# Kernel optimization log

Hardware: AMD Instinct MI355X
Metric: run time of the kernel (lower is better)

The kernel has to match this reference:

```python
import jax, jax.numpy as jnp
import numpy as np

N = 100_000   # nodes
E = 3_200_000 # edges (avg degree 32)
IN = 256      # input feature dim


def setup_inputs() -> dict:
    key = jax.random.key(0)
    ks = jax.random.split(key, 10)
    w = lambda k, s: (jax.random.normal(k, s, jnp.float32) * 0.02)
    return {
        "x": jax.random.normal(ks[0], (N, IN), jnp.float32),
        "edge_index": jax.random.randint(ks[1], (2, E), 0, N, dtype=jnp.int32),
        "edge_attr": jax.random.normal(ks[2], (E, 1), jnp.float32),
        # conv1: ExpGraphConv(IN, 64, 128)
        "W1a": w(ks[3], (IN, 64)), "b1a": jnp.zeros((64,), jnp.float32),
        "W1b": w(ks[4], (IN + 64, 128)), "b1b": jnp.zeros((128,), jnp.float32),
        # conv2: ExpGraphConv(128, 32->hidden 64? per ctor (128, 32, 64)): msg hidden 32... kept as repo: hidden=32? Using (128,64) msg, (192,64) out per faithful cat structure
        "W2a": w(ks[5], (128, 64)), "b2a": jnp.zeros((64,), jnp.float32),
        "W2b": w(ks[6], (128 + 64, 64)), "b2b": jnp.zeros((64,), jnp.float32),
        # head
        "Wl1": w(ks[7], (64, 32)), "bl1": jnp.zeros((32,), jnp.float32),
        "Wl2": w(ks[8], (32, 1)), "bl2": jnp.zeros((1,), jnp.float32),
    }


def _mean_aggr(h, src, dst, n):
    # gather messages from source nodes, scatter-mean into destination nodes
    s = jax.ops.segment_sum(h[src], dst, num_segments=n)          # [N, d]
    cnt = jax.ops.segment_sum(jnp.ones((src.shape[0],), h.dtype), dst, num_segments=n)
    return s / jnp.maximum(cnt, 1.0)[:, None]


def _exp_graph_conv(x, src, dst, Wa, ba, Wb, bb):
    # message MLP on source features, mean aggregation, then linear on [x || aggr]
    h = x @ Wa + ba                                               # [N, hidden]
    m = _mean_aggr(h, src, dst, x.shape[0])                       # [N, hidden]
    return jnp.concatenate([x, m], axis=1) @ Wb + bb              # [N, out]


def reference(x, edge_index, edge_attr, W1a, b1a, W1b, b1b, W2a, b2a, W2b, b2b, Wl1, bl1, Wl2, bl2):
    src, dst = edge_index[0], edge_index[1]
    x = jax.nn.relu(_exp_graph_conv(x, src, dst, W1a, b1a, W1b, b1b))
    x = jax.nn.relu(_exp_graph_conv(x, src, dst, W2a, b2a, W2b, b2b))
    x = jax.nn.relu(x @ Wl1 + bl1)
    return x @ Wl2 + bl2
```

## Files before the change

### kernel.cpp

```cpp
#include <hip/hip_runtime.h>

#define IN_DIM 256
#define CAP 10240
#define EPB 4096

typedef _Float16 f16;
typedef _Float16 f16x8 __attribute__((ext_vector_type(8)));
typedef float f32x4 __attribute__((ext_vector_type(4)));
typedef unsigned u32x4 __attribute__((ext_vector_type(4)));
typedef unsigned u32x2 __attribute__((ext_vector_type(2)));


__global__ __launch_bounds__(256) void bucket_scatter_k(const int* __restrict__ srcp,
                                                        const int* __restrict__ dstp,
                                                        int* __restrict__ bcur,
                                                        unsigned* __restrict__ bedge, int E) {
    __shared__ int cnt[512], lstart[512], delta[512], fill[512];
    __shared__ int pfx[256];
    __shared__ unsigned spay[EPB];
    __shared__ unsigned char sbk[EPB];
    int tid = threadIdx.x;
    cnt[tid] = 0; cnt[tid + 256] = 0;
    fill[tid] = 0; fill[tid + 256] = 0;
    __syncthreads();
    size_t base = (size_t)blockIdx.x * EPB;
    int nloc = E - (int)base; if (nloc > EPB) nloc = EPB;
    int dreg[EPB / 256], sreg[EPB / 256];
#pragma unroll
    for (int j = 0; j < EPB / 256; j++) {
        int e = j * 256 + tid;
        if (e < nloc) {
            dreg[j] = dstp[base + e];
            sreg[j] = srcp[base + e];
            atomicAdd(&cnt[dreg[j] >> 8], 1);
        }
    }
    __syncthreads();
    int a0 = cnt[2 * tid], a1 = cnt[2 * tid + 1], s = a0 + a1;
    pfx[tid] = s;
    __syncthreads();
    for (int off = 1; off < 256; off <<= 1) {
        int t2 = (tid >= off) ? pfx[tid - off] : 0;
        __syncthreads();
        pfx[tid] += t2;
        __syncthreads();
    }
    int excl = pfx[tid] - s;
    lstart[2 * tid] = excl;
    lstart[2 * tid + 1] = excl + a0;
    int g0 = 0, g1 = 0;
    if (a0) g0 = atomicAdd(&bcur[2 * tid], a0);
    if (a1) g1 = atomicAdd(&bcur[2 * tid + 1], a1);
    delta[2 * tid]     = (2 * tid) * CAP + g0 - excl;
    delta[2 * tid + 1] = (2 * tid + 1) * CAP + g1 - (excl + a0);
    __syncthreads();
#pragma unroll
    for (int j = 0; j < EPB / 256; j++) {
        int e = j * 256 + tid;
        if (e < nloc) {
            int d = dreg[j], bk = d >> 8;
            int slot = lstart[bk] + atomicAdd(&fill[bk], 1);
            spay[slot] = (unsigned)sreg[j] | ((unsigned)(d & 255) << 17);
            sbk[slot] = (unsigned char)bk;
        }
    }
    __syncthreads();
    int mid = lstart[256];
#pragma unroll
    for (int j = 0; j < EPB / 256; j++) {
        int i = j * 256 + tid;
        if (i < nloc) {
            int bk = (int)sbk[i] | ((i >= mid) ? 256 : 0);
            int gp = i + delta[bk];
            if (gp < (bk + 1) * CAP)
                bedge[gp] = spay[i];
        }
    }
}

__global__ __launch_bounds__(256) void fine_sort_k(unsigned* __restrict__ bedge,
                                                   const int* __restrict__ bcur,
                                                   int2* __restrict__ ose, int Nn) {
    __shared__ int cnt[256], cur[256], pfx[256];
    __shared__ int sorted[CAP];
    int b = blockIdx.x, tid = threadIdx.x;
    int lo = b * CAP;
    int sz = bcur[b];
    if (sz > CAP) sz = CAP;
    cnt[tid] = 0;
    __syncthreads();
    for (int i = tid; i < sz; i += 256) atomicAdd(&cnt[bedge[lo + i] >> 17], 1);
    __syncthreads();
    int c = cnt[tid];
    pfx[tid] = c;
    __syncthreads();
    for (int off = 1; off < 256; off <<= 1) {
        int t2 = (tid >= off) ? pfx[tid - off] : 0;
        __syncthreads();
        pfx[tid] += t2;
        __syncthreads();
    }
    int excl = pfx[tid] - c;
    cur[tid] = excl;
    int node = b * 256 + tid;
    if (node < Nn) ose[node] = make_int2(lo + excl, lo + excl + c);
    __syncthreads();
    for (int i = tid; i < sz; i += 256) {
        unsigned v = bedge[lo + i];
        int slot = atomicAdd(&cur[v >> 17], 1);
        sorted[slot] = (int)(v & 0x1FFFFu);
    }
    __syncthreads();
    for (int i = tid; i < sz; i += 256) bedge[lo + i] = (unsigned)sorted[i];
}


__global__ __launch_bounds__(256) void prep_k(
    const float* __restrict__ W1a, const float* __restrict__ W1b,
    const float* __restrict__ W2a, const float* __restrict__ W2b,
    const float* __restrict__ b1a, const float* __restrict__ b1b,
    const float* __restrict__ b2a, const float* __restrict__ b2b,
    f16* __restrict__ Wt1, f16* __restrict__ Wt2,
    f16* __restrict__ Wmt1, f16* __restrict__ Wmt2,
    float* __restrict__ bc1, float* __restrict__ bc2,
    int* __restrict__ bcur) {
    int tid = threadIdx.x;
    if (blockIdx.x == 0) { bcur[tid] = 0; bcur[tid + 256] = 0; }
    int i = blockIdx.x * 256 + tid;
    if (i < 49152) {
        int n = i >> 8, k = i & 255;
        Wt1[i] = (f16)(n < 64 ? W1a[k * 64 + n] : W1b[k * 128 + (n - 64)]);
    } else if (i < 65536) {
        int l = i - 49152; int n = l >> 7, k = l & 127;
        Wt2[l] = (f16)(n < 64 ? W2a[k * 64 + n] : W2b[k * 64 + (n - 64)]);
    } else if (i < 73728) {
        int l = i - 65536; int n = l >> 6, k = l & 63;
        Wmt1[l] = (f16)W1b[(256 + k) * 128 + n];
    } else if (i < 77824) {
        int l = i - 73728; int n = l >> 6, k = l & 63;
        Wmt2[l] = (f16)W2b[(128 + k) * 64 + n];
    } else if (i < 78016) {
        int l = i - 77824; bc1[l] = l < 64 ? b1a[l] : b1b[l - 64];
    } else if (i < 78144) {
        int l = i - 78016; bc2[l] = l < 64 ? b2a[l] : b2b[l - 64];
    }
}


__global__ __launch_bounds__(256) void gemm_fused192(const float* __restrict__ A1,
                                                     const f16* __restrict__ Wt,
                                                     const float* __restrict__ bc,
                                                     f16* __restrict__ Y1,
                                                     f16* __restrict__ Y2, int M) {
    constexpr int BN = 192, BM = 64, BK = 32, ASTR = BK + 8, K1 = 256;
    constexpr int WN = BN / 2, NB = WN / 16, SEGB = BN / 64;
    constexpr int EPS = BN + 8, TPR = BN / 8;
    constexpr size_t SM_AB = (size_t)BM * ASTR * 2 + (size_t)BN * ASTR * 2;
    constexpr size_t SM_EP = (size_t)BM * EPS * 2;
    constexpr size_t SM = SM_AB > SM_EP ? SM_AB : SM_EP;
    __shared__ __align__(16) char smem[SM];
    f16* As = reinterpret_cast<f16*>(smem);
    f16* Bs = reinterpret_cast<f16*>(smem + (size_t)BM * ASTR * 2);
    const int tid  = threadIdx.x;
    const int wave = tid >> 6, lane = tid & 63;
    const int wr = wave >> 1, wc = wave & 1;
    const int quad = lane >> 4, l16 = lane & 15;
    const int row0 = blockIdx.x * BM;

    f32x4 acc[2][NB];
#pragma unroll
    for (int i = 0; i < 2; i++)
#pragma unroll
        for (int j = 0; j < NB; j++) acc[i][j] = (f32x4)(0.f);

    const int ra = tid >> 2, sa = tid & 3;
    int rowA = row0 + ra;  if (rowA >= M) rowA = M - 1;

    u32x4 aReg, bReg[SEGB];
    auto loadA = [&](int kk) {
        const float* bp = A1 + (size_t)rowA * K1 + kk + sa * 8;
        f32x4 v0 = __builtin_nontemporal_load(reinterpret_cast<const f32x4*>(bp));
        f32x4 v1 = __builtin_nontemporal_load(reinterpret_cast<const f32x4*>(bp) + 1);
        union { f16 h[8]; u32x4 u; } p;
        p.h[0] = (f16)v0.x; p.h[1] = (f16)v0.y; p.h[2] = (f16)v0.z; p.h[3] = (f16)v0.w;
        p.h[4] = (f16)v1.x; p.h[5] = (f16)v1.y; p.h[6] = (f16)v1.z; p.h[7] = (f16)v1.w;
        aReg = p.u;
    };
    auto loadB = [&](int kk) {
#pragma unroll
        for (int i = 0; i < SEGB; i++) {
            int fid = tid + i * 256;
            int n = fid >> 2, s = fid & 3;
            bReg[i] = *reinterpret_cast<const u32x4*>(Wt + (size_t)n * K1 + kk + s * 8);
        }
    };

    loadA(0); loadB(0);
    for (int kk = 0; kk < K1; kk += BK) {
        *reinterpret_cast<u32x4*>(&As[ra * ASTR + sa * 8]) = aReg;
#pragma unroll
        for (int i = 0; i < SEGB; i++) {
            int fid = tid + i * 256;
            int n = fid >> 2, s = fid & 3;
            *reinterpret_cast<u32x4*>(&Bs[n * ASTR + s * 8]) = bReg[i];
        }
        __syncthreads();
        if (kk + BK < K1) { loadA(kk + BK); loadB(kk + BK); }
        f16x8 af[2], bf[NB];
#pragma unroll
        for (int rb = 0; rb < 2; rb++) {
            int row = wr * 32 + rb * 16 + l16;
            af[rb] = *reinterpret_cast<const f16x8*>(&As[row * ASTR + quad * 8]);
        }
#pragma unroll
        for (int cb = 0; cb < NB; cb++) {
            int n = wc * WN + cb * 16 + l16;
            bf[cb] = *reinterpret_cast<const f16x8*>(&Bs[n * ASTR + quad * 8]);
        }
#pragma unroll
        for (int rb = 0; rb < 2; rb++)
#pragma unroll
            for (int cb = 0; cb < NB; cb++)
                acc[rb][cb] = __builtin_amdgcn_mfma_f32_16x16x32_f16(af[rb], bf[cb], acc[rb][cb], 0, 0, 0);
        __syncthreads();
    }

    f16* ep = reinterpret_cast<f16*>(smem);
#pragma unroll
    for (int rb = 0; rb < 2; rb++) {
#pragma unroll
        for (int cb = 0; cb < NB; cb++) {
            int col = wc * WN + cb * 16 + l16;
            float bv = bc[col];
#pragma unroll
            for (int r = 0; r < 4; r++) {
                int lrow = wr * 32 + rb * 16 + quad * 4 + r;
                ep[(size_t)lrow * EPS + col] = (f16)(acc[rb][cb][r] + bv);
            }
        }
    }
    __syncthreads();
#pragma unroll
    for (int p = 0; p < BM * TPR / 256; p++) {
        int fid = p * 256 + tid;
        int row = fid / TPR, c = fid % TPR, col0 = c * 8;
        int grow = row0 + row;
        if (grow < M) {
            u32x4 val = *reinterpret_cast<const u32x4*>(&ep[(size_t)row * EPS + col0]);
            if (col0 < 64)
                *reinterpret_cast<u32x4*>(Y1 + (size_t)grow * 64 + col0) = val;
            else
                __builtin_nontemporal_store(val,
                    reinterpret_cast<u32x4*>(Y2 + (size_t)grow * 128 + (col0 - 64)));
        }
    }
}


__global__ __launch_bounds__(256) void aggr_k(const int2* __restrict__ ose,
                                              const int* __restrict__ ssrc,
                                              const f16* __restrict__ h,
                                              f16* __restrict__ m, int n) {
    int wave = (blockIdx.x * 256 + threadIdx.x) >> 6;
    int lane = threadIdx.x & 63;
    if (wave >= n) return;
    int2 se = ose[wave];
    int s0 = se.x, s1 = se.y;
    const int l8 = lane & 7;
    const int r8 = lane >> 3;
    const u32x4* hp = reinterpret_cast<const u32x4*>(h);
    float a0 = 0.f, a1 = 0.f, a2 = 0.f, a3 = 0.f;
    float a4 = 0.f, a5 = 0.f, a6 = 0.f, a7 = 0.f;
    auto accum = [&](u32x4 u) {
        union { u32x4 u; f16 hh[8]; } p; p.u = u;
        a0 += (float)p.hh[0]; a1 += (float)p.hh[1];
        a2 += (float)p.hh[2]; a3 += (float)p.hh[3];
        a4 += (float)p.hh[4]; a5 += (float)p.hh[5];
        a6 += (float)p.hh[6]; a7 += (float)p.hh[7];
    };
    for (int c = s0; c < s1; c += 64) {
        int cn = min(64, s1 - c);
        int myidx = (lane < cn) ? ssrc[c + lane] : 0;
        int t = 0;
        for (; t + 16 <= cn; t += 16) {
            int ia = __shfl(myidx, t + r8);
            int ib = __shfl(myidx, t + 8 + r8);
            u32x4 ua = hp[(size_t)ia * 8 + l8];
            u32x4 ub = hp[(size_t)ib * 8 + l8];
            accum(ua); accum(ub);
        }
        if (t + 8 <= cn) {
            int ia = __shfl(myidx, t + r8);
            accum(hp[(size_t)ia * 8 + l8]);
            t += 8;
        }
        if (t < cn) {
            int r = t + r8;
            int rr = (r < cn) ? r : (cn - 1);
            int ia = __shfl(myidx, rr);
            if (r < cn) accum(hp[(size_t)ia * 8 + l8]);
        }
    }
#define RED(d) a0 += __shfl_xor(a0, d); a1 += __shfl_xor(a1, d); \
               a2 += __shfl_xor(a2, d); a3 += __shfl_xor(a3, d); \
               a4 += __shfl_xor(a4, d); a5 += __shfl_xor(a5, d); \
               a6 += __shfl_xor(a6, d); a7 += __shfl_xor(a7, d);
    RED(8) RED(16) RED(32)
#undef RED
    if (lane < 8) {
        float inv = 1.0f / fmaxf((float)(s1 - s0), 1.0f);
        union { u32x4 u; f16 hh[8]; } pk;
        pk.hh[0] = (f16)(a0 * inv); pk.hh[1] = (f16)(a1 * inv);
        pk.hh[2] = (f16)(a2 * inv); pk.hh[3] = (f16)(a3 * inv);
        pk.hh[4] = (f16)(a4 * inv); pk.hh[5] = (f16)(a5 * inv);
        pk.hh[6] = (f16)(a6 * inv); pk.hh[7] = (f16)(a7 * inv);
        reinterpret_cast<u32x4*>(m + (size_t)wave * 64)[l8] = pk.u;
    }
}


__global__ __launch_bounds__(256) void comb_gemm_k(const f16* __restrict__ Mb,
                                                   const f16* __restrict__ Wmt,
                                                   const f16* __restrict__ P,
                                                   const f16* __restrict__ Wt2,
                                                   const float* __restrict__ bc2,
                                                   f16* __restrict__ H2,
                                                   f16* __restrict__ P2,
                                                   int M) {
    constexpr int BM = 64, ASTR = 72, TSTR = 136, BSTR = 40;
    constexpr int BN1 = 128, NB1 = 4;
    constexpr int NB2c = 4;
    __shared__ __align__(16) char smem[27648];
    f16* As  = reinterpret_cast<f16*>(smem);
    f16* Bs1 = reinterpret_cast<f16*>(smem + (size_t)BM * ASTR * 2);
    f16* tile = reinterpret_cast<f16*>(smem);
    f16* Bs2 = reinterpret_cast<f16*>(smem + (size_t)BM * TSTR * 2);
    const int tid  = threadIdx.x;
    const int wave = tid >> 6, lane = tid & 63;
    const int wr = wave >> 1, wc = wave & 1;
    const int quad = lane >> 4, l16 = lane & 15;
    const int row0 = blockIdx.x * BM;

#pragma unroll
    for (int fid = tid; fid < 512; fid += 256) {
        int row = fid >> 3, s = fid & 7;
        int grow = row0 + row; if (grow >= M) grow = M - 1;
        *reinterpret_cast<u32x4*>(&As[row * ASTR + s * 8]) =
            *reinterpret_cast<const u32x4*>(Mb + (size_t)grow * 64 + s * 8);
    }
#pragma unroll
    for (int fid = tid; fid < BN1 * 8; fid += 256) {
        int n = fid >> 3, s = fid & 7;
        *reinterpret_cast<u32x4*>(&Bs1[n * ASTR + s * 8]) =
            *reinterpret_cast<const u32x4*>(Wmt + (size_t)n * 64 + s * 8);
    }
    __syncthreads();

    f32x4 acc[2][NB1];
#pragma unroll
    for (int i = 0; i < 2; i++)
#pragma unroll
        for (int j = 0; j < NB1; j++) acc[i][j] = (f32x4)(0.f);
#pragma unroll
    for (int ks = 0; ks < 2; ks++) {
        f16x8 af[2], bf[NB1];
#pragma unroll
        for (int rb = 0; rb < 2; rb++) {
            int row = wr * 32 + rb * 16 + l16;
            af[rb] = *reinterpret_cast<const f16x8*>(&As[row * ASTR + ks * 32 + quad * 8]);
        }
#pragma unroll
        for (int cb = 0; cb < NB1; cb++) {
            int n = wc * 64 + cb * 16 + l16;
            bf[cb] = *reinterpret_cast<const f16x8*>(&Bs1[n * ASTR + ks * 32 + quad * 8]);
        }
#pragma unroll
        for (int rb = 0; rb < 2; rb++)
#pragma unroll
            for (int cb = 0; cb < NB1; cb++)
                acc[rb][cb] = __builtin_amdgcn_mfma_f32_16x16x32_f16(af[rb], bf[cb], acc[rb][cb], 0, 0, 0);
    }
    __syncthreads();

#pragma unroll
    for (int rb = 0; rb < 2; rb++) {
#pragma unroll
        for (int cb = 0; cb < NB1; cb++) {
            int col = wc * 64 + cb * 16 + l16;
#pragma unroll
            for (int r = 0; r < 4; r++) {
                int lrow = wr * 32 + rb * 16 + quad * 4 + r;
                int grow = row0 + lrow;
                float pv = (grow < M) ? (float)P[(size_t)grow * 128 + col] : 0.f;
                tile[(size_t)lrow * TSTR + col] = (f16)fmaxf(acc[rb][cb][r] + pv, 0.f);
            }
        }
    }

    f32x4 acc2[2][NB2c];
#pragma unroll
    for (int i = 0; i < 2; i++)
#pragma unroll
        for (int j = 0; j < NB2c; j++) acc2[i][j] = (f32x4)(0.f);

    u32x4 bReg[2];
    auto loadB2 = [&](int kk) {
#pragma unroll
        for (int i = 0; i < 2; i++) {
            int fid = tid + i * 256;
            int n = fid >> 2, s = fid & 3;
            bReg[i] = *reinterpret_cast<const u32x4*>(Wt2 + (size_t)n * 128 + kk + s * 8);
        }
    };
    loadB2(0);
    for (int kk = 0; kk < 128; kk += 32) {
#pragma unroll
        for (int i = 0; i < 2; i++) {
            int fid = tid + i * 256;
            int n = fid >> 2, s = fid & 3;
            *reinterpret_cast<u32x4*>(&Bs2[n * BSTR + s * 8]) = bReg[i];
        }
        __syncthreads();
        if (kk + 32 < 128) loadB2(kk + 32);
        f16x8 af[2], bf[NB2c];
#pragma unroll
        for (int rb = 0; rb < 2; rb++) {
            int row = wr * 32 + rb * 16 + l16;
            af[rb] = *reinterpret_cast<const f16x8*>(&tile[(size_t)row * TSTR + kk + quad * 8]);
        }
#pragma unroll
        for (int cb = 0; cb < NB2c; cb++) {
            int n = wc * 64 + cb * 16 + l16;
            bf[cb] = *reinterpret_cast<const f16x8*>(&Bs2[n * BSTR + quad * 8]);
        }
#pragma unroll
        for (int rb = 0; rb < 2; rb++)
#pragma unroll
            for (int cb = 0; cb < NB2c; cb++)
                acc2[rb][cb] = __builtin_amdgcn_mfma_f32_16x16x32_f16(af[rb], bf[cb], acc2[rb][cb], 0, 0, 0);
        __syncthreads();
    }

    f16* ep = tile;
#pragma unroll
    for (int rb = 0; rb < 2; rb++) {
#pragma unroll
        for (int cb = 0; cb < NB2c; cb++) {
            int col = wc * 64 + cb * 16 + l16;
            float bv = bc2[col];
#pragma unroll
            for (int r = 0; r < 4; r++) {
                int lrow = wr * 32 + rb * 16 + quad * 4 + r;
                ep[(size_t)lrow * TSTR + col] = (f16)(acc2[rb][cb][r] + bv);
            }
        }
    }
    __syncthreads();
#pragma unroll
    for (int p = 0; p < 4; p++) {
        int fid = p * 256 + tid;
        int row = fid >> 4, c = fid & 15, col0 = c * 8;
        int grow = row0 + row;
        if (grow < M) {
            u32x4 val = *reinterpret_cast<const u32x4*>(&ep[(size_t)row * TSTR + col0]);
            if (col0 < 64)
                *reinterpret_cast<u32x4*>(H2 + (size_t)grow * 64 + col0) = val;
            else
                __builtin_nontemporal_store(val,
                    reinterpret_cast<u32x4*>(P2 + (size_t)grow * 64 + (col0 - 64)));
        }
    }
}


__global__ __launch_bounds__(256) void comb_head_k(const f16* __restrict__ Mb,
                                                   const f16* __restrict__ Wmt,
                                                   const f16* __restrict__ P,
                                                   const float* __restrict__ Wl1,
                                                   const float* __restrict__ bl1,
                                                   const float* __restrict__ Wl2,
                                                   const float* __restrict__ bl2,
                                                   float* __restrict__ out, int M) {
    constexpr int BM = 64, ASTR = 72, BN = 64, NB = 2;
    constexpr int EPS = BN + 8;
    constexpr size_t SZ_A = (size_t)BM * ASTR * 2;
    constexpr size_t SM_AB = SZ_A + (size_t)BN * ASTR * 2;
    constexpr size_t SM_EP = (size_t)BM * EPS * 2;
    constexpr size_t SM_CORE = SM_AB > SM_EP ? SM_AB : SM_EP;
    __shared__ __align__(16) char smem[SM_CORE + (2048 + 64) * 4];
    f16* As = reinterpret_cast<f16*>(smem);
    f16* Bs = reinterpret_cast<f16*>(smem + SZ_A);
    const int tid  = threadIdx.x;
    const int wave = tid >> 6, lane = tid & 63;
    const int wr = wave >> 1, wc = wave & 1;
    const int quad = lane >> 4, l16 = lane & 15;
    const int row0 = blockIdx.x * BM;

#pragma unroll
    for (int fid = tid; fid < 512; fid += 256) {
        int row = fid >> 3, s = fid & 7;
        int grow = row0 + row; if (grow >= M) grow = M - 1;
        *reinterpret_cast<u32x4*>(&As[row * ASTR + s * 8]) =
            *reinterpret_cast<const u32x4*>(Mb + (size_t)grow * 64 + s * 8);
    }
    for (int fid = tid; fid < BN * 8; fid += 256) {
        int n = fid >> 3, s = fid & 7;
        *reinterpret_cast<u32x4*>(&Bs[n * ASTR + s * 8]) =
            *reinterpret_cast<const u32x4*>(Wmt + (size_t)n * 64 + s * 8);
    }
    {
        float* w1s = reinterpret_cast<float*>(smem + SM_CORE);
        for (int t2 = tid; t2 < 2048; t2 += 256) w1s[t2] = Wl1[t2];
        if (tid < 32) { w1s[2048 + tid] = bl1[tid]; w1s[2048 + 32 + tid] = Wl2[tid]; }
    }
    __syncthreads();

    f32x4 acc[2][NB];
#pragma unroll
    for (int i = 0; i < 2; i++)
#pragma unroll
        for (int j = 0; j < NB; j++) acc[i][j] = (f32x4)(0.f);
#pragma unroll
    for (int ks = 0; ks < 2; ks++) {
        f16x8 af[2], bf[NB];
#pragma unroll
        for (int rb = 0; rb < 2; rb++) {
            int row = wr * 32 + rb * 16 + l16;
            af[rb] = *reinterpret_cast<const f16x8*>(&As[row * ASTR + ks * 32 + quad * 8]);
        }
#pragma unroll
        for (int cb = 0; cb < NB; cb++) {
            int n = wc * 32 + cb * 16 + l16;
            bf[cb] = *reinterpret_cast<const f16x8*>(&Bs[n * ASTR + ks * 32 + quad * 8]);
        }
#pragma unroll
        for (int rb = 0; rb < 2; rb++)
#pragma unroll
            for (int cb = 0; cb < NB; cb++)
                acc[rb][cb] = __builtin_amdgcn_mfma_f32_16x16x32_f16(af[rb], bf[cb], acc[rb][cb], 0, 0, 0);
    }
    __syncthreads();

    f16* ep = reinterpret_cast<f16*>(smem);
#pragma unroll
    for (int rb = 0; rb < 2; rb++) {
#pragma unroll
        for (int cb = 0; cb < NB; cb++) {
            int col = wc * 32 + cb * 16 + l16;
#pragma unroll
            for (int r = 0; r < 4; r++) {
                int lrow = wr * 32 + rb * 16 + quad * 4 + r;
                int grow = row0 + lrow;
                float pv = (grow < M) ? (float)P[(size_t)grow * 64 + col] : 0.f;
                ep[(size_t)lrow * EPS + col] = (f16)fmaxf(acc[rb][cb][r] + pv, 0.f);
            }
        }
    }
    __syncthreads();

    float* w1s = reinterpret_cast<float*>(smem + SM_CORE);
    float* b1s = w1s + 2048;
    float* w2s = b1s + 32;
    int row = tid >> 2, part = tid & 3;
    const f16* eprow = ep + (size_t)row * EPS;
    float hj[8];
#pragma unroll
    for (int j = 0; j < 8; j++) hj[j] = b1s[part * 8 + j];
    for (int k = 0; k < 64; k++) {
        float v = (float)eprow[k];
        const float* wrow = &w1s[k * 32 + part * 8];
#pragma unroll
        for (int j = 0; j < 8; j++) hj[j] += v * wrow[j];
    }
    float o = 0.f;
#pragma unroll
    for (int j = 0; j < 8; j++) o += fmaxf(hj[j], 0.f) * w2s[part * 8 + j];
    o += __shfl_xor(o, 1);
    o += __shfl_xor(o, 2);
    int grow = row0 + row;
    if (part == 0 && grow < M) out[grow] = o + bl2[0];
}


extern "C" void kernel_launch(void* const* d_in, const int* in_sizes, int n_in,
                              void* d_out, int out_size, void* d_ws, size_t ws_size,
                              hipStream_t stream) {
    const float* x   = (const float*)d_in[0];
    const int*   ei  = (const int*)d_in[1];
    const float* W1a = (const float*)d_in[3];
    const float* b1a = (const float*)d_in[4];
    const float* W1b = (const float*)d_in[5];
    const float* b1b = (const float*)d_in[6];
    const float* W2a = (const float*)d_in[7];
    const float* b2a = (const float*)d_in[8];
    const float* W2b = (const float*)d_in[9];
    const float* b2b = (const float*)d_in[10];
    const float* Wl1 = (const float*)d_in[11];
    const float* bl1 = (const float*)d_in[12];
    const float* Wl2 = (const float*)d_in[13];
    const float* bl2 = (const float*)d_in[14];

    const int N = in_sizes[0] / IN_DIM;
    const int E = in_sizes[1] / 2;
    const int* srcp = ei;
    const int* dstp = ei + E;

    char* ws = (char*)d_ws;
    size_t off = 0;
    auto alloc = [&](size_t bytes) -> char* {
        char* p = ws + off;
        off = (off + bytes + 255) & ~(size_t)255;
        return p;
    };
    int NB2 = (N + 255) / 256;
    int*      bcur  = (int*)alloc(512 * 4);
    unsigned* bedge = (unsigned*)alloc((size_t)NB2 * CAP * 4);
    int2*     ose   = (int2*)alloc((size_t)N * 8);
    f16*      hbuf  = (f16*)alloc((size_t)N * 64 * 2);
    f16*      mbuf  = (f16*)alloc((size_t)N * 64 * 2);
    f16*      pbuf  = (f16*)alloc((size_t)N * 128 * 2);
    f16*      h2    = (f16*)alloc((size_t)N * 64 * 2);
    f16*      p2    = (f16*)alloc((size_t)N * 64 * 2);
    f16*      Wt1   = (f16*)alloc(192 * 256 * 2);
    f16*      Wt2   = (f16*)alloc(128 * 128 * 2);
    f16*      Wmt1  = (f16*)alloc(128 * 64 * 2);
    f16*      Wmt2  = (f16*)alloc(64 * 64 * 2);
    float*    bc1   = (float*)alloc(192 * 4);
    float*    bc2   = (float*)alloc(128 * 4);
    (void)ws_size;

    prep_k<<<306, 256, 0, stream>>>(W1a, W1b, W2a, W2b, b1a, b1b, b2a, b2b,
                                    Wt1, Wt2, Wmt1, Wmt2, bc1, bc2, bcur);
    int ebk = (E + EPB - 1) / EPB;
    bucket_scatter_k<<<ebk, 256, 0, stream>>>(srcp, dstp, bcur, bedge, E);
    fine_sort_k<<<NB2, 256, 0, stream>>>(bedge, bcur, ose, N);

    int mb = (N + 63) / 64;
    int ab = (N * 64 + 255) / 256;
    const int* ssrc = (const int*)bedge;

    gemm_fused192<<<mb, 256, 0, stream>>>(x, Wt1, bc1, hbuf, pbuf, N);
    aggr_k<<<ab, 256, 0, stream>>>(ose, ssrc, hbuf, mbuf, N);
    comb_gemm_k<<<mb, 256, 0, stream>>>(mbuf, Wmt1, pbuf, Wt2, bc2, h2, p2, N);

    aggr_k<<<ab, 256, 0, stream>>>(ose, ssrc, h2, mbuf, N);
    comb_head_k<<<mb, 256, 0, stream>>>(mbuf, Wmt2, p2, Wl1, bl1, Wl2, bl2,
                                        (float*)d_out, N);
}
```

Baseline: 436.0 us.

## Co-schedule edge bucketing with first GEMM and fuse second aggregation into head

Merges the edge bucket-scatter and the first fused GEMM into one launch, with blocks split by index, so the independent bucketing work overlaps the layer-1 GEMM and one launch is saved. The second mean aggregation is folded into the final combine/head kernel: each 1024-thread block aggregates 16 nodes with one wave per node into shared memory, then runs the MFMA combine and the MLP head. This removes the mbuf round trip and a launch. The cost is low MFMA utilisation in the head (16 rows per block, only 4 of 16 waves doing matrix work) and larger blocks that may limit occupancy.

```diff
diff --git a/kernel.cpp b/kernel.cpp
--- a/kernel.cpp
+++ b/kernel.cpp
@@ -9,110 +9,6 @@
 typedef float f32x4 __attribute__((ext_vector_type(4)));
 typedef unsigned u32x4 __attribute__((ext_vector_type(4)));
 typedef unsigned u32x2 __attribute__((ext_vector_type(2)));
-
-
-__global__ __launch_bounds__(256) void bucket_scatter_k(const int* __restrict__ srcp,
-                                                        const int* __restrict__ dstp,
-                                                        int* __restrict__ bcur,
-                                                        unsigned* __restrict__ bedge, int E) {
-    __shared__ int cnt[512], lstart[512], delta[512], fill[512];
-    __shared__ int pfx[256];
-    __shared__ unsigned spay[EPB];
-    __shared__ unsigned char sbk[EPB];
-    int tid = threadIdx.x;
-    cnt[tid] = 0; cnt[tid + 256] = 0;
-    fill[tid] = 0; fill[tid + 256] = 0;
-    __syncthreads();
-    size_t base = (size_t)blockIdx.x * EPB;
-    int nloc = E - (int)base; if (nloc > EPB) nloc = EPB;
-    int dreg[EPB / 256], sreg[EPB / 256];
-#pragma unroll
-    for (int j = 0; j < EPB / 256; j++) {
-        int e = j * 256 + tid;
-        if (e < nloc) {
-            dreg[j] = dstp[base + e];
-            sreg[j] = srcp[base + e];
-            atomicAdd(&cnt[dreg[j] >> 8], 1);
-        }
-    }
-    __syncthreads();
-    int a0 = cnt[2 * tid], a1 = cnt[2 * tid + 1], s = a0 + a1;
-    pfx[tid] = s;
-    __syncthreads();
-    for (int off = 1; off < 256; off <<= 1) {
-        int t2 = (tid >= off) ? pfx[tid - off] : 0;
-        __syncthreads();
-        pfx[tid] += t2;
-        __syncthreads();
-    }
-    int excl = pfx[tid] - s;
-    lstart[2 * tid] = excl;
-    lstart[2 * tid + 1] = excl + a0;
-    int g0 = 0, g1 = 0;
-    if (a0) g0 = atomicAdd(&bcur[2 * tid], a0);
-    if (a1) g1 = atomicAdd(&bcur[2 * tid + 1], a1);
-    delta[2 * tid]     = (2 * tid) * CAP + g0 - excl;
-    delta[2 * tid + 1] = (2 * tid + 1) * CAP + g1 - (excl + a0);
-    __syncthreads();
-#pragma unroll
-    for (int j = 0; j < EPB / 256; j++) {
-        int e = j * 256 + tid;
-        if (e < nloc) {
-            int d = dreg[j], bk = d >> 8;
-            int slot = lstart[bk] + atomicAdd(&fill[bk], 1);
-            spay[slot] = (unsigned)sreg[j] | ((unsigned)(d & 255) << 17);
-            sbk[slot] = (unsigned char)bk;
-        }
-    }
-    __syncthreads();
-    int mid = lstart[256];
-#pragma unroll
-    for (int j = 0; j < EPB / 256; j++) {
-        int i = j * 256 + tid;
-        if (i < nloc) {
-            int bk = (int)sbk[i] | ((i >= mid) ? 256 : 0);
-            int gp = i + delta[bk];
-            if (gp < (bk + 1) * CAP)
-                bedge[gp] = spay[i];
-        }
-    }
-}
-
-__global__ __launch_bounds__(256) void fine_sort_k(unsigned* __restrict__ bedge,
-                                                   const int* __restrict__ bcur,
-                                                   int2* __restrict__ ose, int Nn) {
-    __shared__ int cnt[256], cur[256], pfx[256];
-    __shared__ int sorted[CAP];
-    int b = blockIdx.x, tid = threadIdx.x;
-    int lo = b * CAP;
-    int sz = bcur[b];
-    if (sz > CAP) sz = CAP;
-    cnt[tid] = 0;
-    __syncthreads();
-    for (int i = tid; i < sz; i += 256) atomicAdd(&cnt[bedge[lo + i] >> 17], 1);
-    __syncthreads();
-    int c = cnt[tid];
-    pfx[tid] = c;
-    __syncthreads();
-    for (int off = 1; off < 256; off <<= 1) {
-        int t2 = (tid >= off) ? pfx[tid - off] : 0;
-        __syncthreads();
-        pfx[tid] += t2;
-        __syncthreads();
-    }
-    int excl = pfx[tid] - c;
-    cur[tid] = excl;
-    int node = b * 256 + tid;
-    if (node < Nn) ose[node] = make_int2(lo + excl, lo + excl + c);
-    __syncthreads();
-    for (int i = tid; i < sz; i += 256) {
-        unsigned v = bedge[lo + i];
-        int slot = atomicAdd(&cur[v >> 17], 1);
-        sorted[slot] = (int)(v & 0x1FFFFu);
-    }
-    __syncthreads();
-    for (int i = tid; i < sz; i += 256) bedge[lo + i] = (unsigned)sorted[i];
-}
 
 
 __global__ __launch_bounds__(256) void prep_k(
@@ -147,25 +43,92 @@
 }
 
 
-__global__ __launch_bounds__(256) void gemm_fused192(const float* __restrict__ A1,
-                                                     const f16* __restrict__ Wt,
-                                                     const float* __restrict__ bc,
-                                                     f16* __restrict__ Y1,
-                                                     f16* __restrict__ Y2, int M) {
+__global__ __launch_bounds__(256) void fat_k(
+    const int* __restrict__ srcp, const int* __restrict__ dstp,
+    int* __restrict__ bcur, unsigned* __restrict__ bedge, int E, int ebk,
+    const float* __restrict__ A1, const f16* __restrict__ Wt,
+    const float* __restrict__ bc, f16* __restrict__ Y1,
+    f16* __restrict__ Y2, int M) {
+    __shared__ __align__(16) char sm[29696];
+    const int tid = threadIdx.x;
+
+    if ((int)blockIdx.x < ebk) {
+        int* cnt    = reinterpret_cast<int*>(sm);
+        int* lstart = cnt + 512;
+        int* delta  = lstart + 512;
+        int* fill   = delta + 512;
+        int* pfx    = fill + 512;
+        unsigned* spay = reinterpret_cast<unsigned*>(pfx + 256);
+        unsigned char* sbk = reinterpret_cast<unsigned char*>(spay + EPB);
+        cnt[tid] = 0; cnt[tid + 256] = 0;
+        fill[tid] = 0; fill[tid + 256] = 0;
+        __syncthreads();
+        size_t base = (size_t)blockIdx.x * EPB;
+        int nloc = E - (int)base; if (nloc > EPB) nloc = EPB;
+        int dreg[EPB / 256], sreg[EPB / 256];
+#pragma unroll
+        for (int j = 0; j < EPB / 256; j++) {
+            int e = j * 256 + tid;
+            if (e < nloc) {
+                dreg[j] = dstp[base + e];
+                sreg[j] = srcp[base + e];
+                atomicAdd(&cnt[dreg[j] >> 8], 1);
+            }
+        }
+        __syncthreads();
+        int a0 = cnt[2 * tid], a1 = cnt[2 * tid + 1], s = a0 + a1;
+        pfx[tid] = s;
+        __syncthreads();
+        for (int off = 1; off < 256; off <<= 1) {
+            int t2 = (tid >= off) ? pfx[tid - off] : 0;
+            __syncthreads();
+            pfx[tid] += t2;
+            __syncthreads();
+        }
+        int excl = pfx[tid] - s;
+        lstart[2 * tid] = excl;
+        lstart[2 * tid + 1] = excl + a0;
+        int g0 = 0, g1 = 0;
+        if (a0) g0 = atomicAdd(&bcur[2 * tid], a0);
+        if (a1) g1 = atomicAdd(&bcur[2 * tid + 1], a1);
+        delta[2 * tid]     = (2 * tid) * CAP + g0 - excl;
+        delta[2 * tid + 1] = (2 * tid + 1) * CAP + g1 - (excl + a0);
+        __syncthreads();
+#pragma unroll
+        for (int j = 0; j < EPB / 256; j++) {
+            int e = j * 256 + tid;
+            if (e < nloc) {
+                int d = dreg[j], bk = d >> 8;
+                int slot = lstart[bk] + atomicAdd(&fill[bk], 1);
+                spay[slot] = (unsigned)sreg[j] | ((unsigned)(d & 255) << 17);
+                sbk[slot] = (unsigned char)bk;
+            }
+        }
+        __syncthreads();
+        int mid = lstart[256];
+#pragma unroll
+        for (int j = 0; j < EPB / 256; j++) {
+            int i = j * 256 + tid;
+            if (i < nloc) {
+                int bk = (int)sbk[i] | ((i >= mid) ? 256 : 0);
+                int gp = i + delta[bk];
+                if (gp < (bk + 1) * CAP)
+                    bedge[gp] = spay[i];
+            }
+        }
+        return;
+    }
+
     constexpr int BN = 192, BM = 64, BK = 32, ASTR = BK + 8, K1 = 256;
     constexpr int WN = BN / 2, NB = WN / 16, SEGB = BN / 64;
     constexpr int EPS = BN + 8, TPR = BN / 8;
-    constexpr size_t SM_AB = (size_t)BM * ASTR * 2 + (size_t)BN * ASTR * 2;
-    constexpr size_t SM_EP = (size_t)BM * EPS * 2;
-    constexpr size_t SM = SM_AB > SM_EP ? SM_AB : SM_EP;
-    __shared__ __align__(16) char smem[SM];
-    f16* As = reinterpret_cast<f16*>(smem);
-    f16* Bs = reinterpret_cast<f16*>(smem + (size_t)BM * ASTR * 2);
-    const int tid  = threadIdx.x;
+    f16* As = reinterpret_cast<f16*>(sm);
+    f16* Bs = reinterpret_cast<f16*>(sm + (size_t)BM * ASTR * 2);
+    const int bid  = (int)blockIdx.x - ebk;
     const int wave = tid >> 6, lane = tid & 63;
     const int wr = wave >> 1, wc = wave & 1;
     const int quad = lane >> 4, l16 = lane & 15;
-    const int row0 = blockIdx.x * BM;
+    const int row0 = bid * BM;
 
     f32x4 acc[2][NB];
 #pragma unroll
@@ -225,7 +188,7 @@
         __syncthreads();
     }
 
-    f16* ep = reinterpret_cast<f16*>(smem);
+    f16* ep = reinterpret_cast<f16*>(sm);
 #pragma unroll
     for (int rb = 0; rb < 2; rb++) {
 #pragma unroll
@@ -254,6 +217,43 @@
                     reinterpret_cast<u32x4*>(Y2 + (size_t)grow * 128 + (col0 - 64)));
         }
     }
+}
+
+
+__global__ __launch_bounds__(256) void fine_sort_k(unsigned* __restrict__ bedge,
+                                                   const int* __restrict__ bcur,
+                                                   int2* __restrict__ ose, int Nn) {
+    __shared__ int cnt[256], cur[256], pfx[256];
+    __shared__ int sorted[CAP];
+    int b = blockIdx.x, tid = threadIdx.x;
+    int lo = b * CAP;
+    int sz = bcur[b];
+    if (sz > CAP) sz = CAP;
+    cnt[tid] = 0;
+    __syncthreads();
+    for (int i = tid; i < sz; i += 256) atomicAdd(&cnt[bedge[lo + i] >> 17], 1);
+    __syncthreads();
+    int c = cnt[tid];
+    pfx[tid] = c;
+    __syncthreads();
+    for (int off = 1; off < 256; off <<= 1) {
+        int t2 = (tid >= off) ? pfx[tid - off] : 0;
+        __syncthreads();
+        pfx[tid] += t2;
+        __syncthreads();
+    }
+    int excl = pfx[tid] - c;
+    cur[tid] = excl;
+    int node = b * 256 + tid;
+    if (node < Nn) ose[node] = make_int2(lo + excl, lo + excl + c);
+    __syncthreads();
+    for (int i = tid; i < sz; i += 256) {
+        unsigned v = bedge[lo + i];
+        int slot = atomicAdd(&cur[v >> 17], 1);
+        sorted[slot] = (int)(v & 0x1FFFFu);
+    }
+    __syncthreads();
+    for (int i = tid; i < sz; i += 256) bedge[lo + i] = (unsigned)sorted[i];
 }
 
 
@@ -473,112 +473,130 @@
 }
 
 
-__global__ __launch_bounds__(256) void comb_head_k(const f16* __restrict__ Mb,
+__global__ __launch_bounds__(1024, 8) void mega2_k(const int2* __restrict__ ose,
+                                                   const int* __restrict__ ssrc,
+                                                   const f16* __restrict__ h,
                                                    const f16* __restrict__ Wmt,
                                                    const f16* __restrict__ P,
                                                    const float* __restrict__ Wl1,
                                                    const float* __restrict__ bl1,
                                                    const float* __restrict__ Wl2,
                                                    const float* __restrict__ bl2,
-                                                   float* __restrict__ out, int M) {
-    constexpr int BM = 64, ASTR = 72, BN = 64, NB = 2;
-    constexpr int EPS = BN + 8;
-    constexpr size_t SZ_A = (size_t)BM * ASTR * 2;
-    constexpr size_t SM_AB = SZ_A + (size_t)BN * ASTR * 2;
-    constexpr size_t SM_EP = (size_t)BM * EPS * 2;
-    constexpr size_t SM_CORE = SM_AB > SM_EP ? SM_AB : SM_EP;
-    __shared__ __align__(16) char smem[SM_CORE + (2048 + 64) * 4];
-    f16* As = reinterpret_cast<f16*>(smem);
-    f16* Bs = reinterpret_cast<f16*>(smem + SZ_A);
-    const int tid  = threadIdx.x;
-    const int wave = tid >> 6, lane = tid & 63;
-    const int wr = wave >> 1, wc = wave & 1;
-    const int quad = lane >> 4, l16 = lane & 15;
-    const int row0 = blockIdx.x * BM;
-
-#pragma unroll
-    for (int fid = tid; fid < 512; fid += 256) {
-        int row = fid >> 3, s = fid & 7;
-        int grow = row0 + row; if (grow >= M) grow = M - 1;
-        *reinterpret_cast<u32x4*>(&As[row * ASTR + s * 8]) =
-            *reinterpret_cast<const u32x4*>(Mb + (size_t)grow * 64 + s * 8);
-    }
-    for (int fid = tid; fid < BN * 8; fid += 256) {
-        int n = fid >> 3, s = fid & 7;
-        *reinterpret_cast<u32x4*>(&Bs[n * ASTR + s * 8]) =
-            *reinterpret_cast<const u32x4*>(Wmt + (size_t)n * 64 + s * 8);
-    }
+                                                   float* __restrict__ out, int n) {
+    constexpr int ASTR = 72, EPS = 72;
+    __shared__ __align__(16) f16 Am[16 * ASTR];
+    __shared__ __align__(16) f16 Bs[64 * ASTR];
+    __shared__ __align__(16) f16 ep[16 * EPS];
+    __shared__ float w1s[2048];
+    __shared__ float b1s[32], w2s[32];
+    const int tid = threadIdx.x;
+    const int wv = tid >> 6, lane = tid & 63;
+    const int row0 = blockIdx.x * 16;
+
+    for (int fid = tid; fid < 512; fid += 1024) {
+        int nn = fid >> 3, s = fid & 7;
+        *reinterpret_cast<u32x4*>(&Bs[nn * ASTR + s * 8]) =
+            *reinterpret_cast<const u32x4*>(Wmt + (size_t)nn * 64 + s * 8);
+    }
+    for (int i = tid; i < 2048; i += 1024) w1s[i] = Wl1[i];
+    if (tid < 32) { b1s[tid] = bl1[tid]; w2s[tid] = Wl2[tid]; }
+
     {
-        float* w1s = reinterpret_cast<float*>(smem + SM_CORE);
-        for (int t2 = tid; t2 < 2048; t2 += 256) w1s[t2] = Wl1[t2];
-        if (tid < 32) { w1s[2048 + tid] = bl1[tid]; w1s[2048 + 32 + tid] = Wl2[tid]; }
-    }
-    __syncthreads();
-
-    f32x4 acc[2][NB];
-#pragma unroll
-    for (int i = 0; i < 2; i++)
-#pragma unroll
-        for (int j = 0; j < NB; j++) acc[i][j] = (f32x4)(0.f);
-#pragma unroll
-    for (int ks = 0; ks < 2; ks++) {
-        f16x8 af[2], bf[NB];
-#pragma unroll
-        for (int rb = 0; rb < 2; rb++) {
-            int row = wr * 32 + rb * 16 + l16;
-            af[rb] = *reinterpret_cast<const f16x8*>(&As[row * ASTR + ks * 32 + quad * 8]);
-        }
-#pragma unroll
-        for (int cb = 0; cb < NB; cb++) {
-            int n = wc * 32 + cb * 16 + l16;
-            bf[cb] = *reinterpret_cast<const f16x8*>(&Bs[n * ASTR + ks * 32 + quad * 8]);
-        }
-#pragma unroll
-        for (int rb = 0; rb < 2; rb++)
-#pragma unroll
-            for (int cb = 0; cb < NB; cb++)
-                acc[rb][cb] = __builtin_amdgcn_mfma_f32_16x16x32_f16(af[rb], bf[cb], acc[rb][cb], 0, 0, 0);
-    }
-    __syncthreads();
-
-    f16* ep = reinterpret_cast<f16*>(smem);
-#pragma unroll
-    for (int rb = 0; rb < 2; rb++) {
-#pragma unroll
-        for (int cb = 0; cb < NB; cb++) {
-            int col = wc * 32 + cb * 16 + l16;
-#pragma unroll
-            for (int r = 0; r < 4; r++) {
-                int lrow = wr * 32 + rb * 16 + quad * 4 + r;
-                int grow = row0 + lrow;
-                float pv = (grow < M) ? (float)P[(size_t)grow * 64 + col] : 0.f;
-                ep[(size_t)lrow * EPS + col] = (f16)fmaxf(acc[rb][cb][r] + pv, 0.f);
-            }
-        }
-    }
-    __syncthreads();
-
-    float* w1s = reinterpret_cast<float*>(smem + SM_CORE);
-    float* b1s = w1s + 2048;
-    float* w2s = b1s + 32;
-    int row = tid >> 2, part = tid & 3;
-    const f16* eprow = ep + (size_t)row * EPS;
-    float hj[8];
-#pragma unroll
-    for (int j = 0; j < 8; j++) hj[j] = b1s[part * 8 + j];
-    for (int k = 0; k < 64; k++) {
-        float v = (float)eprow[k];
-        const float* wrow = &w1s[k * 32 + part * 8];
-#pragma unroll
-        for (int j = 0; j < 8; j++) hj[j] += v * wrow[j];
-    }
-    float o = 0.f;
-#pragma unroll
-    for (int j = 0; j < 8; j++) o += fmaxf(hj[j], 0.f) * w2s[part * 8 + j];
-    o += __shfl_xor(o, 1);
-    o += __shfl_xor(o, 2);
-    int grow = row0 + row;
-    if (part == 0 && grow < M) out[grow] = o + bl2[0];
+        int node = row0 + wv;
+        int2 se = (node < n) ? ose[node] : make_int2(0, 0);
+        int s0 = se.x, s1 = se.y;
+        const int l8 = lane & 7;
+        const int r8 = lane >> 3;
+        const u32x4* hp = reinterpret_cast<const u32x4*>(h);
+        float a0 = 0.f, a1 = 0.f, a2 = 0.f, a3 = 0.f;
+        float a4 = 0.f, a5 = 0.f, a6 = 0.f, a7 = 0.f;
+        auto accum = [&](u32x4 u) {
+            union { u32x4 u; f16 hh[8]; } p; p.u = u;
+            a0 += (float)p.hh[0]; a1 += (float)p.hh[1];
+            a2 += (float)p.hh[2]; a3 += (float)p.hh[3];
+            a4 += (float)p.hh[4]; a5 += (float)p.hh[5];
+            a6 += (float)p.hh[6]; a7 += (float)p.hh[7];
+        };
+        for (int c = s0; c < s1; c += 64) {
+            int cn = min(64, s1 - c);
+            int myidx = (lane < cn) ? ssrc[c + lane] : 0;
+            int t = 0;
+            for (; t + 16 <= cn; t += 16) {
+                int ia = __shfl(myidx, t + r8);
+                int ib = __shfl(myidx, t + 8 + r8);
+                u32x4 ua = hp[(size_t)ia * 8 + l8];
+                u32x4 ub = hp[(size_t)ib * 8 + l8];
+                accum(ua); accum(ub);
+            }
+            if (t + 8 <= cn) {
+                int ia = __shfl(myidx, t + r8);
+                accum(hp[(size_t)ia * 8 + l8]);
+                t += 8;
+            }
+            if (t < cn) {
+                int r = t + r8;
+                int rr = (r < cn) ? r : (cn - 1);
+                int ia = __shfl(myidx, rr);
+                if (r < cn) accum(hp[(size_t)ia * 8 + l8]);
+            }
+        }
+#define RED(d) a0 += __shfl_xor(a0, d); a1 += __shfl_xor(a1, d); \
+               a2 += __shfl_xor(a2, d); a3 += __shfl_xor(a3, d); \
+               a4 += __shfl_xor(a4, d); a5 += __shfl_xor(a5, d); \
+               a6 += __shfl_xor(a6, d); a7 += __shfl_xor(a7, d);
+        RED(8) RED(16) RED(32)
+#undef RED
+        if (lane < 8) {
+            float inv = 1.0f / fmaxf((float)(s1 - s0), 1.0f);
+            union { u32x4 u; f16 hh[8]; } pk;
+            pk.hh[0] = (f16)(a0 * inv); pk.hh[1] = (f16)(a1 * inv);
+            pk.hh[2] = (f16)(a2 * inv); pk.hh[3] = (f16)(a3 * inv);
+            pk.hh[4] = (f16)(a4 * inv); pk.hh[5] = (f16)(a5 * inv);
+            pk.hh[6] = (f16)(a6 * inv); pk.hh[7] = (f16)(a7 * inv);
+            *reinterpret_cast<u32x4*>(&Am[wv * ASTR + l8 * 8]) = pk.u;
+        }
+    }
+    __syncthreads();
+
+    if (wv < 4) {
+        const int quad = lane >> 4, l16 = lane & 15;
+        f32x4 acc = (f32x4)(0.f);
+#pragma unroll
+        for (int ks = 0; ks < 2; ks++) {
+            f16x8 af = *reinterpret_cast<const f16x8*>(&Am[l16 * ASTR + ks * 32 + quad * 8]);
+            f16x8 bf = *reinterpret_cast<const f16x8*>(&Bs[(wv * 16 + l16) * ASTR + ks * 32 + quad * 8]);
+            acc = __builtin_amdgcn_mfma_f32_16x16x32_f16(af, bf, acc, 0, 0, 0);
+        }
+#pragma unroll
+        for (int r = 0; r < 4; r++) {
+            int lrow = quad * 4 + r;
+            int grow = row0 + lrow;
+            float pv = (grow < n) ? (float)P[(size_t)grow * 64 + wv * 16 + l16] : 0.f;
+            ep[lrow * EPS + wv * 16 + l16] = (f16)fmaxf(acc[r] + pv, 0.f);
+        }
+    }
+    __syncthreads();
+
+    if (tid < 64) {
+        int row = tid >> 2, part = tid & 3;
+        const f16* eprow = ep + (size_t)row * EPS;
+        float hj[8];
+#pragma unroll
+        for (int j = 0; j < 8; j++) hj[j] = b1s[part * 8 + j];
+        for (int k = 0; k < 64; k++) {
+            float v = (float)eprow[k];
+            const float* wrow = &w1s[k * 32 + part * 8];
+#pragma unroll
+            for (int j = 0; j < 8; j++) hj[j] += v * wrow[j];
+        }
+        float o = 0.f;
+#pragma unroll
+        for (int j = 0; j < 8; j++) o += fmaxf(hj[j], 0.f) * w2s[part * 8 + j];
+        o += __shfl_xor(o, 1);
+        o += __shfl_xor(o, 2);
+        int grow = row0 + row;
+        if (part == 0 && grow < n) out[grow] = o + bl2[0];
+    }
 }
 
 
@@ -629,21 +647,21 @@
     float*    bc2   = (float*)alloc(128 * 4);
     (void)ws_size;
 
+    int mb  = (N + 63) / 64;
+    int ab  = (N * 64 + 255) / 256;
+    int ebk = (E + EPB - 1) / EPB;
+    const int* ssrc = (const int*)bedge;
+
     prep_k<<<306, 256, 0, stream>>>(W1a, W1b, W2a, W2b, b1a, b1b, b2a, b2b,
                                     Wt1, Wt2, Wmt1, Wmt2, bc1, bc2, bcur);
-    int ebk = (E + EPB - 1) / EPB;
-    bucket_scatter_k<<<ebk, 256, 0, stream>>>(srcp, dstp, bcur, bedge, E);
+    fat_k<<<ebk + mb, 256, 0, stream>>>(srcp, dstp, bcur, bedge, E, ebk,
+                                        x, Wt1, bc1, hbuf, pbuf, N);
     fine_sort_k<<<NB2, 256, 0, stream>>>(bedge, bcur, ose, N);
 
-    int mb = (N + 63) / 64;
-    int ab = (N * 64 + 255) / 256;
-    const int* ssrc = (const int*)bedge;
-
-    gemm_fused192<<<mb, 256, 0, stream>>>(x, Wt1, bc1, hbuf, pbuf, N);
     aggr_k<<<ab, 256, 0, stream>>>(ose, ssrc, hbuf, mbuf, N);
     comb_gemm_k<<<mb, 256, 0, stream>>>(mbuf, Wmt1, pbuf, Wt2, bc2, h2, p2, N);
 
-    aggr_k<<<ab, 256, 0, stream>>>(ose, ssrc, h2, mbuf, N);
-    comb_head_k<<<mb, 256, 0, stream>>>(mbuf, Wmt2, p2, Wl1, bl1, Wl2, bl2,
-                                        (float*)d_out, N);
+    mega2_k<<<(N + 15) / 16, 1024, 0, stream>>>(ose, ssrc, h2, Wmt2, p2,
+                                                Wl1, bl1, Wl2, bl2,
+                                                (float*)d_out, N);
 }
```

New measurement: 475.0 us. 9.0% more time.

## Merge edge bucket scatter and first fused GEMM into one heterogeneous launch

Applied to the files above, without the earlier changes.

Combines the edge bucket-scatter kernel and the first-layer fused GEMM into a single kernel. The first ebk blocks do the scatter and the remaining blocks do the GEMM tiles, with shared memory sized to cover both roles. The two independent phases can then run concurrently on the GPU and one launch gap goes away. In exchange, both roles share one register and LDS footprint, which may reduce occupancy for each. Fine sort now runs after the GEMM has finished.

```diff
diff --git a/kernel.cpp b/kernel.cpp
--- a/kernel.cpp
+++ b/kernel.cpp
@@ -9,110 +9,6 @@
 typedef float f32x4 __attribute__((ext_vector_type(4)));
 typedef unsigned u32x4 __attribute__((ext_vector_type(4)));
 typedef unsigned u32x2 __attribute__((ext_vector_type(2)));
-
-
-__global__ __launch_bounds__(256) void bucket_scatter_k(const int* __restrict__ srcp,
-                                                        const int* __restrict__ dstp,
-                                                        int* __restrict__ bcur,
-                                                        unsigned* __restrict__ bedge, int E) {
-    __shared__ int cnt[512], lstart[512], delta[512], fill[512];
-    __shared__ int pfx[256];
-    __shared__ unsigned spay[EPB];
-    __shared__ unsigned char sbk[EPB];
-    int tid = threadIdx.x;
-    cnt[tid] = 0; cnt[tid + 256] = 0;
-    fill[tid] = 0; fill[tid + 256] = 0;
-    __syncthreads();
-    size_t base = (size_t)blockIdx.x * EPB;
-    int nloc = E - (int)base; if (nloc > EPB) nloc = EPB;
-    int dreg[EPB / 256], sreg[EPB / 256];
-#pragma unroll
-    for (int j = 0; j < EPB / 256; j++) {
-        int e = j * 256 + tid;
-        if (e < nloc) {
-            dreg[j] = dstp[base + e];
-            sreg[j] = srcp[base + e];
-            atomicAdd(&cnt[dreg[j] >> 8], 1);
-        }
-    }
-    __syncthreads();
-    int a0 = cnt[2 * tid], a1 = cnt[2 * tid + 1], s = a0 + a1;
-    pfx[tid] = s;
-    __syncthreads();
-    for (int off = 1; off < 256; off <<= 1) {
-        int t2 = (tid >= off) ? pfx[tid - off] : 0;
-        __syncthreads();
-        pfx[tid] += t2;
-        __syncthreads();
-    }
-    int excl = pfx[tid] - s;
-    lstart[2 * tid] = excl;
-    lstart[2 * tid + 1] = excl + a0;
-    int g0 = 0, g1 = 0;
-    if (a0) g0 = atomicAdd(&bcur[2 * tid], a0);
-    if (a1) g1 = atomicAdd(&bcur[2 * tid + 1], a1);
-    delta[2 * tid]     = (2 * tid) * CAP + g0 - excl;
-    delta[2 * tid + 1] = (2 * tid + 1) * CAP + g1 - (excl + a0);
-    __syncthreads();
-#pragma unroll
-    for (int j = 0; j < EPB / 256; j++) {
-        int e = j * 256 + tid;
-        if (e < nloc) {
-            int d = dreg[j], bk = d >> 8;
-            int slot = lstart[bk] + atomicAdd(&fill[bk], 1);
-            spay[slot] = (unsigned)sreg[j] | ((unsigned)(d & 255) << 17);
-            sbk[slot] = (unsigned char)bk;
-        }
-    }
-    __syncthreads();
-    int mid = lstart[256];
-#pragma unroll
-    for (int j = 0; j < EPB / 256; j++) {
-        int i = j * 256 + tid;
-        if (i < nloc) {
-            int bk = (int)sbk[i] | ((i >= mid) ? 256 : 0);
-            int gp = i + delta[bk];
-            if (gp < (bk + 1) * CAP)
-                bedge[gp] = spay[i];
-        }
-    }
-}
-
-__global__ __launch_bounds__(256) void fine_sort_k(unsigned* __restrict__ bedge,
-                                                   const int* __restrict__ bcur,
-                                                   int2* __restrict__ ose, int Nn) {
-    __shared__ int cnt[256], cur[256], pfx[256];
-    __shared__ int sorted[CAP];
-    int b = blockIdx.x, tid = threadIdx.x;
-    int lo = b * CAP;
-    int sz = bcur[b];
-    if (sz > CAP) sz = CAP;
-    cnt[tid] = 0;
-    __syncthreads();
-    for (int i = tid; i < sz; i += 256) atomicAdd(&cnt[bedge[lo + i] >> 17], 1);
-    __syncthreads();
-    int c = cnt[tid];
-    pfx[tid] = c;
-    __syncthreads();
-    for (int off = 1; off < 256; off <<= 1) {
-        int t2 = (tid >= off) ? pfx[tid - off] : 0;
-        __syncthreads();
-        pfx[tid] += t2;
-        __syncthreads();
-    }
-    int excl = pfx[tid] - c;
-    cur[tid] = excl;
-    int node = b * 256 + tid;
-    if (node < Nn) ose[node] = make_int2(lo + excl, lo + excl + c);
-    __syncthreads();
-    for (int i = tid; i < sz; i += 256) {
-        unsigned v = bedge[lo + i];
-        int slot = atomicAdd(&cur[v >> 17], 1);
-        sorted[slot] = (int)(v & 0x1FFFFu);
-    }
-    __syncthreads();
-    for (int i = tid; i < sz; i += 256) bedge[lo + i] = (unsigned)sorted[i];
-}
 
 
 __global__ __launch_bounds__(256) void prep_k(
@@ -147,25 +43,92 @@
 }
 
 
-__global__ __launch_bounds__(256) void gemm_fused192(const float* __restrict__ A1,
-                                                     const f16* __restrict__ Wt,
-                                                     const float* __restrict__ bc,
-                                                     f16* __restrict__ Y1,
-                                                     f16* __restrict__ Y2, int M) {
+__global__ __launch_bounds__(256) void fat_k(
+    const int* __restrict__ srcp, const int* __restrict__ dstp,
+    int* __restrict__ bcur, unsigned* __restrict__ bedge, int E, int ebk,
+    const float* __restrict__ A1, const f16* __restrict__ Wt,
+    const float* __restrict__ bc, f16* __restrict__ Y1,
+    f16* __restrict__ Y2, int M) {
+    __shared__ __align__(16) char sm[29696];
+    const int tid = threadIdx.x;
+
+    if ((int)blockIdx.x < ebk) {
+        int* cnt    = reinterpret_cast<int*>(sm);
+        int* lstart = cnt + 512;
+        int* delta  = lstart + 512;
+        int* fill   = delta + 512;
+        int* pfx    = fill + 512;
+        unsigned* spay = reinterpret_cast<unsigned*>(pfx + 256);
+        unsigned char* sbk = reinterpret_cast<unsigned char*>(spay + EPB);
+        cnt[tid] = 0; cnt[tid + 256] = 0;
+        fill[tid] = 0; fill[tid + 256] = 0;
+        __syncthreads();
+        size_t base = (size_t)blockIdx.x * EPB;
+        int nloc = E - (int)base; if (nloc > EPB) nloc = EPB;
+        int dreg[EPB / 256], sreg[EPB / 256];
+#pragma unroll
+        for (int j = 0; j < EPB / 256; j++) {
+            int e = j * 256 + tid;
+            if (e < nloc) {
+                dreg[j] = dstp[base + e];
+                sreg[j] = srcp[base + e];
+                atomicAdd(&cnt[dreg[j] >> 8], 1);
+            }
+        }
+        __syncthreads();
+        int a0 = cnt[2 * tid], a1 = cnt[2 * tid + 1], s = a0 + a1;
+        pfx[tid] = s;
+        __syncthreads();
+        for (int off = 1; off < 256; off <<= 1) {
+            int t2 = (tid >= off) ? pfx[tid - off] : 0;
+            __syncthreads();
+            pfx[tid] += t2;
+            __syncthreads();
+        }
+        int excl = pfx[tid] - s;
+        lstart[2 * tid] = excl;
+        lstart[2 * tid + 1] = excl + a0;
+        int g0 = 0, g1 = 0;
+        if (a0) g0 = atomicAdd(&bcur[2 * tid], a0);
+        if (a1) g1 = atomicAdd(&bcur[2 * tid + 1], a1);
+        delta[2 * tid]     = (2 * tid) * CAP + g0 - excl;
+        delta[2 * tid + 1] = (2 * tid + 1) * CAP + g1 - (excl + a0);
+        __syncthreads();
+#pragma unroll
+        for (int j = 0; j < EPB / 256; j++) {
+            int e = j * 256 + tid;
+            if (e < nloc) {
+                int d = dreg[j], bk = d >> 8;
+                int slot = lstart[bk] + atomicAdd(&fill[bk], 1);
+                spay[slot] = (unsigned)sreg[j] | ((unsigned)(d & 255) << 17);
+                sbk[slot] = (unsigned char)bk;
+            }
+        }
+        __syncthreads();
+        int mid = lstart[256];
+#pragma unroll
+        for (int j = 0; j < EPB / 256; j++) {
+            int i = j * 256 + tid;
+            if (i < nloc) {
+                int bk = (int)sbk[i] | ((i >= mid) ? 256 : 0);
+                int gp = i + delta[bk];
+                if (gp < (bk + 1) * CAP)
+                    bedge[gp] = spay[i];
+            }
+        }
+        return;
+    }
+
     constexpr int BN = 192, BM = 64, BK = 32, ASTR = BK + 8, K1 = 256;
     constexpr int WN = BN / 2, NB = WN / 16, SEGB = BN / 64;
     constexpr int EPS = BN + 8, TPR = BN / 8;
-    constexpr size_t SM_AB = (size_t)BM * ASTR * 2 + (size_t)BN * ASTR * 2;
-    constexpr size_t SM_EP = (size_t)BM * EPS * 2;
-    constexpr size_t SM = SM_AB > SM_EP ? SM_AB : SM_EP;
-    __shared__ __align__(16) char smem[SM];
-    f16* As = reinterpret_cast<f16*>(smem);
-    f16* Bs = reinterpret_cast<f16*>(smem + (size_t)BM * ASTR * 2);
-    const int tid  = threadIdx.x;
+    f16* As = reinterpret_cast<f16*>(sm);
+    f16* Bs = reinterpret_cast<f16*>(sm + (size_t)BM * ASTR * 2);
+    const int bid  = (int)blockIdx.x - ebk;
     const int wave = tid >> 6, lane = tid & 63;
     const int wr = wave >> 1, wc = wave & 1;
     const int quad = lane >> 4, l16 = lane & 15;
-    const int row0 = blockIdx.x * BM;
+    const int row0 = bid * BM;
 
     f32x4 acc[2][NB];
 #pragma unroll
@@ -225,7 +188,7 @@
         __syncthreads();
     }
 
-    f16* ep = reinterpret_cast<f16*>(smem);
+    f16* ep = reinterpret_cast<f16*>(sm);
 #pragma unroll
     for (int rb = 0; rb < 2; rb++) {
 #pragma unroll
@@ -254,6 +217,43 @@
                     reinterpret_cast<u32x4*>(Y2 + (size_t)grow * 128 + (col0 - 64)));
         }
     }
+}
+
+
+__global__ __launch_bounds__(256) void fine_sort_k(unsigned* __restrict__ bedge,
+                                                   const int* __restrict__ bcur,
+                                                   int2* __restrict__ ose, int Nn) {
+    __shared__ int cnt[256], cur[256], pfx[256];
+    __shared__ int sorted[CAP];
+    int b = blockIdx.x, tid = threadIdx.x;
+    int lo = b * CAP;
+    int sz = bcur[b];
+    if (sz > CAP) sz = CAP;
+    cnt[tid] = 0;
+    __syncthreads();
+    for (int i = tid; i < sz; i += 256) atomicAdd(&cnt[bedge[lo + i] >> 17], 1);
+    __syncthreads();
+    int c = cnt[tid];
+    pfx[tid] = c;
+    __syncthreads();
+    for (int off = 1; off < 256; off <<= 1) {
+        int t2 = (tid >= off) ? pfx[tid - off] : 0;
+        __syncthreads();
+        pfx[tid] += t2;
+        __syncthreads();
+    }
+    int excl = pfx[tid] - c;
+    cur[tid] = excl;
+    int node = b * 256 + tid;
+    if (node < Nn) ose[node] = make_int2(lo + excl, lo + excl + c);
+    __syncthreads();
+    for (int i = tid; i < sz; i += 256) {
+        unsigned v = bedge[lo + i];
+        int slot = atomicAdd(&cur[v >> 17], 1);
+        sorted[slot] = (int)(v & 0x1FFFFu);
+    }
+    __syncthreads();
+    for (int i = tid; i < sz; i += 256) bedge[lo + i] = (unsigned)sorted[i];
 }
 
 
@@ -629,17 +629,17 @@
     float*    bc2   = (float*)alloc(128 * 4);
     (void)ws_size;
 
+    int mb  = (N + 63) / 64;
+    int ab  = (N * 64 + 255) / 256;
+    int ebk = (E + EPB - 1) / EPB;
+    const int* ssrc = (const int*)bedge;
+
     prep_k<<<306, 256, 0, stream>>>(W1a, W1b, W2a, W2b, b1a, b1b, b2a, b2b,
                                     Wt1, Wt2, Wmt1, Wmt2, bc1, bc2, bcur);
-    int ebk = (E + EPB - 1) / EPB;
-    bucket_scatter_k<<<ebk, 256, 0, stream>>>(srcp, dstp, bcur, bedge, E);
+    fat_k<<<ebk + mb, 256, 0, stream>>>(srcp, dstp, bcur, bedge, E, ebk,
+                                        x, Wt1, bc1, hbuf, pbuf, N);
     fine_sort_k<<<NB2, 256, 0, stream>>>(bedge, bcur, ose, N);
 
-    int mb = (N + 63) / 64;
-    int ab = (N * 64 + 255) / 256;
-    const int* ssrc = (const int*)bedge;
-
-    gemm_fused192<<<mb, 256, 0, stream>>>(x, Wt1, bc1, hbuf, pbuf, N);
     aggr_k<<<ab, 256, 0, stream>>>(ose, ssrc, hbuf, mbuf, N);
     comb_gemm_k<<<mb, 256, 0, stream>>>(mbuf, Wmt1, pbuf, Wt2, bc2, h2, p2, N);
 
```

New measurement: 437.8 us. Within noise of the previous version (+0.4%).
